# Kernel tuning notes

Measured on AMD Instinct MI355X. Metric: run time of the kernel, lower is better.

## Reference

```python
import jax, jax.numpy as jnp
import numpy as np

N_NODES = 100000
N_EDGES = 1600000
IN_F = 128
HID_F = 128
OUT_F = 16
N_GRAPHS = 256


def setup_inputs() -> dict:
    key = jax.random.key(0)
    ks = jax.random.split(key, 6)
    x = jax.random.normal(ks[0], (N_NODES, IN_F), dtype=jnp.float32)
    W1 = jax.random.normal(ks[1], (IN_F, HID_F), dtype=jnp.float32) * (1.0 / np.sqrt(IN_F))
    b1 = jax.random.normal(ks[2], (HID_F,), dtype=jnp.float32) * 0.01
    W2 = jax.random.normal(ks[3], (HID_F, OUT_F), dtype=jnp.float32) * (1.0 / np.sqrt(HID_F))
    b2 = jax.random.normal(ks[4], (OUT_F,), dtype=jnp.float32) * 0.01
    edge_index = jax.random.randint(ks[5], (2, N_EDGES), 0, N_NODES, dtype=jnp.int32)
    # sorted segment ids covering all graphs (~N/G nodes per graph, none empty)
    batch = ((jnp.arange(N_NODES, dtype=jnp.int64) * N_GRAPHS) // N_NODES).astype(jnp.int32)
    return {"x": x, "W1": W1, "b1": b1, "W2": W2, "b2": b2,
            "edge_index": edge_index, "batch": batch, "num_graphs": N_GRAPHS}


def gcn_conv(x, W, b, edge_index):
    # PyG GCNConv: h = x @ W; add self-loops; norm = deg^-1/2[src] * deg^-1/2[dst];
    # out[dst] += norm * h[src]; out += bias
    n = x.shape[0]
    h = x @ W  # [N, H]
    loop = jnp.arange(n, dtype=edge_index.dtype)
    src = jnp.concatenate([edge_index[0], loop])
    dst = jnp.concatenate([edge_index[1], loop])
    deg = jax.ops.segment_sum(jnp.ones_like(dst, dtype=h.dtype), dst, num_segments=n)
    dinv = jnp.where(deg > 0, jax.lax.rsqrt(jnp.maximum(deg, 1.0)), 0.0)
    norm = dinv[src] * dinv[dst]  # [E+N]
    msg = h[src] * norm[:, None]  # gather + scale
    out = jax.ops.segment_sum(msg, dst, num_segments=n)  # scatter-add
    return out + b


def reference(x, W1, b1, W2, b2, edge_index, batch, num_graphs):
    h = gcn_conv(x, W1, b1, edge_index)
    h = jax.nn.relu(h)
    pooled = jax.ops.segment_max(h, batch, num_segments=num_graphs)  # global max pool
    logits = pooled @ W2 + b2
    return jax.nn.log_softmax(logits, axis=-1)
```

## Files before the change

### kernel.cpp

```cpp
#include <hip/hip_runtime.h>

#define N_NODES 100000
#define N_EDGES 1600000
#define FDIM 128
#define OUTF 16
#define NGRAPH 256

#define NBLK 256
#define CHUNK 6250
#define NB_BUCKET 391
#define BC_N (NB_BUCKET * NBLK)
#define BC_SCAN_NB 98

typedef unsigned int uint;
typedef unsigned short ushort;
typedef short bf16x8 __attribute__((ext_vector_type(8)));
typedef float f32x4 __attribute__((ext_vector_type(4)));

__device__ inline uint pack_bf16(float a, float b) {
    uint ua = __float_as_uint(a); ua = (ua + 0x7fffu + ((ua >> 16) & 1u)) >> 16;
    uint ub = __float_as_uint(b); ub = (ub + 0x7fffu + ((ub >> 16) & 1u)) >> 16;
    return ua | (ub << 16);
}
__device__ inline ushort bf16_1(float a) {
    uint u = __float_as_uint(a);
    return (ushort)((u + 0x7fffu + ((u >> 16) & 1u)) >> 16);
}
__device__ inline void unpack_bf16(uint v, float& a, float& b) {
    a = __uint_as_float(v << 16);
    b = __uint_as_float(v & 0xffff0000u);
}

__launch_bounds__(256)
__global__ void k_bhist(const int* __restrict__ dst, int* __restrict__ bcount,
                        float* __restrict__ pooled, int* __restrict__ row_start,
                        const float* __restrict__ W, ushort* __restrict__ wt) {
    __shared__ int hist[NB_BUCKET];
    int t = threadIdx.x, blk = blockIdx.x;
    int gi = blk * 256 + t;
    if (gi < NGRAPH * FDIM) pooled[gi] = 0.0f;
    if (gi < FDIM * FDIM) {
        int col = gi >> 7, k = gi & 127;
        wt[col * 128 + k] = bf16_1(W[k * 128 + col]);
    }
    if (gi == 0) row_start[N_NODES] = N_EDGES;
    for (int i = t; i < NB_BUCKET; i += 256) hist[i] = 0;
    __syncthreads();
    int base = blk * CHUNK;
    for (int j = t; j < CHUNK; j += 256) atomicAdd(&hist[dst[base + j] >> 8], 1);
    __syncthreads();
    for (int i = t; i < NB_BUCKET; i += 256) bcount[i * NBLK + blk] = hist[i];
}

__global__ void k_scan1g(const int* __restrict__ in, int* __restrict__ offs,
                         int* __restrict__ bsums, int n) {
    __shared__ int tmp[256];
    int t = threadIdx.x;
    int base = blockIdx.x * 1024 + t * 4;
    int c[4]; int s = 0;
#pragma unroll
    for (int j = 0; j < 4; ++j) { c[j] = (base + j < n) ? in[base + j] : 0; s += c[j]; }
    tmp[t] = s; __syncthreads();
    for (int off = 1; off < 256; off <<= 1) {
        int v = (t >= off) ? tmp[t - off] : 0;
        __syncthreads();
        tmp[t] += v;
        __syncthreads();
    }
    int run = tmp[t] - s;
#pragma unroll
    for (int j = 0; j < 4; ++j) { if (base + j < n) offs[base + j] = run; run += c[j]; }
    if (t == 255) bsums[blockIdx.x] = tmp[255];
}

__global__ void k_scan2g(int* __restrict__ bsums, int* __restrict__ offs,
                         int nb, int n, int total) {
    if (threadIdx.x == 0) {
        int acc = 0;
        for (int i = 0; i < nb; ++i) { int v = bsums[i]; bsums[i] = acc; acc += v; }
        offs[n] = total;
    }
}

__global__ void k_scan3g(int* __restrict__ offs, const int* __restrict__ bsums, int n) {
    int t = threadIdx.x;
    int base = blockIdx.x * 1024 + t * 4;
    int add = bsums[blockIdx.x];
#pragma unroll
    for (int j = 0; j < 4; ++j) if (base + j < n) offs[base + j] += add;
}

__launch_bounds__(256)
__global__ void k_bucket(const int* __restrict__ src, const int* __restrict__ dst,
                         const int* __restrict__ boff, uint* __restrict__ ebuf) {
    __shared__ int cur[NB_BUCKET];
    int t = threadIdx.x, blk = blockIdx.x;
    for (int i = t; i < NB_BUCKET; i += 256) cur[i] = boff[i * NBLK + blk];
    __syncthreads();
    int base = blk * CHUNK;
    for (int j = t; j < CHUNK; j += 256) {
        int d = dst[base + j], s = src[base + j];
        int pos = atomicAdd(&cur[d >> 8], 1);
        ebuf[pos] = ((uint)(d & 255) << 17) | (uint)s;
    }
}

__launch_bounds__(256)
__global__ void k_build(const uint* __restrict__ ebuf, const int* __restrict__ boff,
                        int* __restrict__ row_start, float* __restrict__ dinv,
                        int* __restrict__ csr_src) {
    __shared__ int cnt[256], sh[256], cur[256];
    int t = threadIdx.x, b = blockIdx.x;
    int bstart = boff[b * NBLK];
    int bend   = boff[(b + 1) * NBLK];
    cnt[t] = 0;
    __syncthreads();
    for (int j = bstart + t; j < bend; j += 256)
        atomicAdd(&cnt[ebuf[j] >> 17], 1);
    __syncthreads();
    int c = cnt[t];
    sh[t] = c;
    __syncthreads();
    for (int o = 1; o < 256; o <<= 1) {
        int v = (t >= o) ? sh[t - o] : 0;
        __syncthreads();
        sh[t] += v;
        __syncthreads();
    }
    int rs = bstart + sh[t] - c;
    cur[t] = rs;
    int node = b * 256 + t;
    if (node < N_NODES) {
        row_start[node] = rs;
        dinv[node] = rsqrtf((float)c + 1.0f);
    }
    __syncthreads();
    for (int j = bstart + t; j < bend; j += 256) {
        uint e = ebuf[j];
        int pos = atomicAdd(&cur[e >> 17], 1);
        csr_src[pos] = (int)(e & 0x1FFFFu);
    }
}

#define BM 128
#define LDP 136
__launch_bounds__(256)
__global__ void k_gemm(const float* __restrict__ x, const ushort* __restrict__ wt,
                       const float* __restrict__ dinv, ushort* __restrict__ hbf) {
    __shared__ ushort AL[BM][LDP];
    __shared__ ushort WL[128][LDP];
    int t = threadIdx.x;
    int r0 = blockIdx.x * BM;

    for (int i = t; i < 128 * 16; i += 256) {
        int r = i >> 4, s = i & 15;
        *(uint4*)&WL[r][s * 8] = *(const uint4*)&wt[r * 128 + s * 8];
    }
    {
        int r = t >> 1, half = t & 1;
        int grow = r0 + r; if (grow >= N_NODES) grow = N_NODES - 1;
        const float4* xp = (const float4*)(x + (long)grow * FDIM + half * 64);
        ushort* ap = &AL[r][half * 64];
#pragma unroll
        for (int i = 0; i < 16; ++i) {
            float4 v = xp[i];
            uint2 p;
            p.x = pack_bf16(v.x, v.y);
            p.y = pack_bf16(v.z, v.w);
            *(uint2*)&ap[i * 4] = p;
        }
    }
    __syncthreads();

    int w = t >> 6, l = t & 63;
    int lr = l & 15;
    int lk = (l >> 4) * 8;
    f32x4 acc[2][8] = {};
#pragma unroll
    for (int kc = 0; kc < 4; ++kc) {
        int ko = kc * 32 + lk;
        bf16x8 a0 = *(const bf16x8*)&AL[w * 32 + lr][ko];
        bf16x8 a1 = *(const bf16x8*)&AL[w * 32 + 16 + lr][ko];
        bf16x8 b[8];
#pragma unroll
        for (int ct = 0; ct < 8; ++ct) b[ct] = *(const bf16x8*)&WL[ct * 16 + lr][ko];
#pragma unroll
        for (int ct = 0; ct < 8; ++ct) {
            acc[0][ct] = __builtin_amdgcn_mfma_f32_16x16x32_bf16(a0, b[ct], acc[0][ct], 0, 0, 0);
            acc[1][ct] = __builtin_amdgcn_mfma_f32_16x16x32_bf16(a1, b[ct], acc[1][ct], 0, 0, 0);
        }
    }
    int rbase = r0 + w * 32 + (l >> 4) * 4;
#pragma unroll
    for (int rt = 0; rt < 2; ++rt) {
#pragma unroll
        for (int reg = 0; reg < 4; ++reg) {
            int row = rbase + rt * 16 + reg;
            if (row < N_NODES) {
                float dv = dinv[row];
#pragma unroll
                for (int ct = 0; ct < 8; ++ct)
                    hbf[(long)row * FDIM + ct * 16 + lr] = bf16_1(dv * acc[rt][ct][reg]);
            }
        }
    }
}

__launch_bounds__(256)
__global__ void k_agg(const ushort* __restrict__ hbf, const float* __restrict__ dinv,
                      const int* __restrict__ row_start, const int* __restrict__ csr_src,
                      const float* __restrict__ b1, ushort* __restrict__ outbf) {
    int t = threadIdx.x;
    int lane = t & 31;
    int node = blockIdx.x * 8 + (t >> 5);
    const uint2* hb = (const uint2*)hbf;
    uint2 v = hb[node * 32 + lane];
    float s0, s1, s2, s3;
    unpack_bf16(v.x, s0, s1); unpack_bf16(v.y, s2, s3);
    int beg = row_start[node], end = row_start[node + 1];
    int j = beg;
    for (; j + 3 < end; j += 4) {
        uint2 va = hb[csr_src[j] * 32 + lane];
        uint2 vb = hb[csr_src[j + 1] * 32 + lane];
        uint2 vc = hb[csr_src[j + 2] * 32 + lane];
        uint2 vd = hb[csr_src[j + 3] * 32 + lane];
        float a0, a1, a2, a3;
        unpack_bf16(va.x, a0, a1); unpack_bf16(va.y, a2, a3);
        s0 += a0; s1 += a1; s2 += a2; s3 += a3;
        unpack_bf16(vb.x, a0, a1); unpack_bf16(vb.y, a2, a3);
        s0 += a0; s1 += a1; s2 += a2; s3 += a3;
        unpack_bf16(vc.x, a0, a1); unpack_bf16(vc.y, a2, a3);
        s0 += a0; s1 += a1; s2 += a2; s3 += a3;
        unpack_bf16(vd.x, a0, a1); unpack_bf16(vd.y, a2, a3);
        s0 += a0; s1 += a1; s2 += a2; s3 += a3;
    }
    for (; j < end; ++j) {
        uint2 va = hb[csr_src[j] * 32 + lane];
        float a0, a1, a2, a3;
        unpack_bf16(va.x, a0, a1); unpack_bf16(va.y, a2, a3);
        s0 += a0; s1 += a1; s2 += a2; s3 += a3;
    }
    float dd = dinv[node];
    float4 bv = ((const float4*)b1)[lane];
    uint2 o;
    o.x = pack_bf16(dd * s0 + bv.x, dd * s1 + bv.y);
    o.y = pack_bf16(dd * s2 + bv.z, dd * s3 + bv.w);
    ((uint2*)outbf)[node * 32 + lane] = o;
}

#define PNODES 64
__global__ void k_pool2(const ushort* __restrict__ outbf, const int* __restrict__ batch,
                        float* __restrict__ pooled) {
    int f = threadIdx.x;
    int r0 = blockIdx.x * PNODES;
    if (r0 >= N_NODES) return;
    int end = r0 + PNODES; if (end > N_NODES) end = N_NODES;
    float m = 0.0f;
    int gcur = batch[r0];
    for (int i = r0; i < end; ++i) {
        int g = batch[i];
        if (g != gcur) {
            atomicMax((int*)&pooled[gcur * FDIM + f], __float_as_int(m));
            m = 0.0f; gcur = g;
        }
        uint u = outbf[(long)i * FDIM + f];
        m = fmaxf(m, __uint_as_float(u << 16));
    }
    atomicMax((int*)&pooled[gcur * FDIM + f], __float_as_int(m));
}

__global__ void k_head(const float* __restrict__ pooled, const float* __restrict__ W2,
                       const float* __restrict__ b2, float* __restrict__ out) {
    int g = blockIdx.x;
    int lane = threadIdx.x;
    int c = lane & 15;
    float acc = b2[c];
    for (int k = 0; k < FDIM; ++k) acc += pooled[g * FDIM + k] * W2[k * OUTF + c];
    float m = acc;
    for (int off = 1; off < 16; off <<= 1) m = fmaxf(m, __shfl_xor(m, off, 16));
    float s = expf(acc - m);
    for (int off = 1; off < 16; off <<= 1) s += __shfl_xor(s, off, 16);
    if (lane < 16) out[g * OUTF + c] = acc - m - logf(s);
}

extern "C" void kernel_launch(void* const* d_in, const int* in_sizes, int n_in,
                              void* d_out, int out_size, void* d_ws, size_t ws_size,
                              hipStream_t stream) {
    const float* x  = (const float*)d_in[0];
    const float* W1 = (const float*)d_in[1];
    const float* b1 = (const float*)d_in[2];
    const float* W2 = (const float*)d_in[3];
    const float* b2 = (const float*)d_in[4];
    const int* ei   = (const int*)d_in[5];
    const int* batch = (const int*)d_in[6];
    const int* src = ei;
    const int* dst = ei + N_EDGES;
    float* out = (float*)d_out;

    char* ws = (char*)d_ws;
    float*  dinv      = (float*) (ws + 0);
    int*    row_start = (int*)   (ws + 400000);
    float*  pooled    = (float*) (ws + 800064);
    int*    bcount    = (int*)   (ws + 931200);
    int*    boff      = (int*)   (ws + 1331648);
    int*    bsums     = (int*)   (ws + 1732096);
    int*    csr_src   = (int*)   (ws + 1732544);
    uint*   ebuf      = (uint*)  (ws + 8132544);
    ushort* hbf       = (ushort*)(ws + 14532544);
    ushort* outbf     = (ushort*)(ws + 40132544);
    ushort* wtbf      = (ushort*)(ws + 65732544);

    k_bhist  <<<NBLK, 256, 0, stream>>>(dst, bcount, pooled, row_start, W1, wtbf);
    k_scan1g <<<BC_SCAN_NB, 256, 0, stream>>>(bcount, boff, bsums, BC_N);
    k_scan2g <<<1, 64, 0, stream>>>(bsums, boff, BC_SCAN_NB, BC_N, N_EDGES);
    k_scan3g <<<BC_SCAN_NB, 256, 0, stream>>>(boff, bsums, BC_N);
    k_bucket <<<NBLK, 256, 0, stream>>>(src, dst, boff, ebuf);
    k_build  <<<NB_BUCKET, 256, 0, stream>>>(ebuf, boff, row_start, dinv, csr_src);
    k_gemm   <<<(N_NODES + BM - 1) / BM, 256, 0, stream>>>(x, wtbf, dinv, hbf);
    k_agg    <<<N_NODES / 8, 256, 0, stream>>>(hbf, dinv, row_start, csr_src, b1, outbf);
    k_pool2  <<<(N_NODES + PNODES - 1) / PNODES, FDIM, 0, stream>>>(outbf, batch, pooled);
    k_head   <<<NGRAPH, 64, 0, stream>>>(pooled, W2, b2, out);
}
```

Baseline: 276.1 us.

## Fuse max-pooling into aggregation kernel and widen gather loads to 16 bytes

The aggregation kernel now applies bias and ReLU, stages each block's 16 node rows in shared memory, and does a per-block segmented max followed by atomicMax into pooled. This removes the bf16 intermediate output buffer and the separate pooling kernel launch, along with its global write and read. Each node is now handled by 16 lanes using uint4 (8 bf16) loads instead of 32 lanes using uint2 loads. The cost is more atomics per graph, since blocks cover only 16 nodes, plus a block-wide sync and shared-memory traffic.

```diff
diff --git a/kernel.cpp b/kernel.cpp
--- a/kernel.cpp
+++ b/kernel.cpp
@@ -206,67 +206,86 @@
     }
 }
 
+#define AGN 16
 __launch_bounds__(256)
 __global__ void k_agg(const ushort* __restrict__ hbf, const float* __restrict__ dinv,
                       const int* __restrict__ row_start, const int* __restrict__ csr_src,
-                      const float* __restrict__ b1, ushort* __restrict__ outbf) {
+                      const float* __restrict__ b1, const int* __restrict__ batch,
+                      float* __restrict__ pooled) {
+    __shared__ float P[AGN][FDIM];
+    __shared__ int sb[AGN];
     int t = threadIdx.x;
-    int lane = t & 31;
-    int node = blockIdx.x * 8 + (t >> 5);
-    const uint2* hb = (const uint2*)hbf;
-    uint2 v = hb[node * 32 + lane];
-    float s0, s1, s2, s3;
+    int lane = t & 15;
+    int ni = t >> 4;
+    int r0 = blockIdx.x * AGN;
+    int node = r0 + ni;
+    if (t < AGN) sb[t] = batch[r0 + t];
+
+    const uint4* hb = (const uint4*)hbf;
+    uint4 v = hb[node * 16 + lane];
+    float s0, s1, s2, s3, s4, s5, s6, s7;
     unpack_bf16(v.x, s0, s1); unpack_bf16(v.y, s2, s3);
+    unpack_bf16(v.z, s4, s5); unpack_bf16(v.w, s6, s7);
     int beg = row_start[node], end = row_start[node + 1];
     int j = beg;
     for (; j + 3 < end; j += 4) {
-        uint2 va = hb[csr_src[j] * 32 + lane];
-        uint2 vb = hb[csr_src[j + 1] * 32 + lane];
-        uint2 vc = hb[csr_src[j + 2] * 32 + lane];
-        uint2 vd = hb[csr_src[j + 3] * 32 + lane];
-        float a0, a1, a2, a3;
-        unpack_bf16(va.x, a0, a1); unpack_bf16(va.y, a2, a3);
-        s0 += a0; s1 += a1; s2 += a2; s3 += a3;
-        unpack_bf16(vb.x, a0, a1); unpack_bf16(vb.y, a2, a3);
-        s0 += a0; s1 += a1; s2 += a2; s3 += a3;
-        unpack_bf16(vc.x, a0, a1); unpack_bf16(vc.y, a2, a3);
-        s0 += a0; s1 += a1; s2 += a2; s3 += a3;
-        unpack_bf16(vd.x, a0, a1); unpack_bf16(vd.y, a2, a3);
-        s0 += a0; s1 += a1; s2 += a2; s3 += a3;
+        uint4 va = hb[csr_src[j] * 16 + lane];
+        uint4 vb = hb[csr_src[j + 1] * 16 + lane];
+        uint4 vc = hb[csr_src[j + 2] * 16 + lane];
+        uint4 vd = hb[csr_src[j + 3] * 16 + lane];
+        float a0, a1;
+        unpack_bf16(va.x, a0, a1); s0 += a0; s1 += a1;
+        unpack_bf16(va.y, a0, a1); s2 += a0; s3 += a1;
+        unpack_bf16(va.z, a0, a1); s4 += a0; s5 += a1;
+        unpack_bf16(va.w, a0, a1); s6 += a0; s7 += a1;
+        unpack_bf16(vb.x, a0, a1); s0 += a0; s1 += a1;
+        unpack_bf16(vb.y, a0, a1); s2 += a0; s3 += a1;
+        unpack_bf16(vb.z, a0, a1); s4 += a0; s5 += a1;
+        unpack_bf16(vb.w, a0, a1); s6 += a0; s7 += a1;
+        unpack_bf16(vc.x, a0, a1); s0 += a0; s1 += a1;
+        unpack_bf16(vc.y, a0, a1); s2 += a0; s3 += a1;
+        unpack_bf16(vc.z, a0, a1); s4 += a0; s5 += a1;
+        unpack_bf16(vc.w, a0, a1); s6 += a0; s7 += a1;
+        unpack_bf16(vd.x, a0, a1); s0 += a0; s1 += a1;
+        unpack_bf16(vd.y, a0, a1); s2 += a0; s3 += a1;
+        unpack_bf16(vd.z, a0, a1); s4 += a0; s5 += a1;
+        unpack_bf16(vd.w, a0, a1); s6 += a0; s7 += a1;
     }
     for (; j < end; ++j) {
-        uint2 va = hb[csr_src[j] * 32 + lane];
-        float a0, a1, a2, a3;
-        unpack_bf16(va.x, a0, a1); unpack_bf16(va.y, a2, a3);
-        s0 += a0; s1 += a1; s2 += a2; s3 += a3;
+        uint4 va = hb[csr_src[j] * 16 + lane];
+        float a0, a1;
+        unpack_bf16(va.x, a0, a1); s0 += a0; s1 += a1;
+        unpack_bf16(va.y, a0, a1); s2 += a0; s3 += a1;
+        unpack_bf16(va.z, a0, a1); s4 += a0; s5 += a1;
+        unpack_bf16(va.w, a0, a1); s6 += a0; s7 += a1;
     }
     float dd = dinv[node];
-    float4 bv = ((const float4*)b1)[lane];
-    uint2 o;
-    o.x = pack_bf16(dd * s0 + bv.x, dd * s1 + bv.y);
-    o.y = pack_bf16(dd * s2 + bv.z, dd * s3 + bv.w);
-    ((uint2*)outbf)[node * 32 + lane] = o;
-}
-
-#define PNODES 64
-__global__ void k_pool2(const ushort* __restrict__ outbf, const int* __restrict__ batch,
-                        float* __restrict__ pooled) {
-    int f = threadIdx.x;
-    int r0 = blockIdx.x * PNODES;
-    if (r0 >= N_NODES) return;
-    int end = r0 + PNODES; if (end > N_NODES) end = N_NODES;
-    float m = 0.0f;
-    int gcur = batch[r0];
-    for (int i = r0; i < end; ++i) {
-        int g = batch[i];
-        if (g != gcur) {
-            atomicMax((int*)&pooled[gcur * FDIM + f], __float_as_int(m));
-            m = 0.0f; gcur = g;
+    const float4* b4 = (const float4*)b1;
+    float4 bva = b4[lane * 2], bvb = b4[lane * 2 + 1];
+    float* pr = &P[ni][lane * 8];
+    pr[0] = fmaxf(0.0f, dd * s0 + bva.x);
+    pr[1] = fmaxf(0.0f, dd * s1 + bva.y);
+    pr[2] = fmaxf(0.0f, dd * s2 + bva.z);
+    pr[3] = fmaxf(0.0f, dd * s3 + bva.w);
+    pr[4] = fmaxf(0.0f, dd * s4 + bvb.x);
+    pr[5] = fmaxf(0.0f, dd * s5 + bvb.y);
+    pr[6] = fmaxf(0.0f, dd * s6 + bvb.z);
+    pr[7] = fmaxf(0.0f, dd * s7 + bvb.w);
+    __syncthreads();
+    if (t < FDIM) {
+        float m = 0.0f;
+        int gcur = sb[0];
+#pragma unroll
+        for (int i = 0; i < AGN; ++i) {
+            int g = sb[i];
+            if (g != gcur) {
+                atomicMax((int*)&pooled[gcur * FDIM + t], __float_as_int(m));
+                m = 0.0f; gcur = g;
+            }
+            m = fmaxf(m, P[i][t]);
         }
-        uint u = outbf[(long)i * FDIM + f];
-        m = fmaxf(m, __uint_as_float(u << 16));
-    }
-    atomicMax((int*)&pooled[gcur * FDIM + f], __float_as_int(m));
+        atomicMax((int*)&pooled[gcur * FDIM + t], __float_as_int(m));
+    }
 }
 
 __global__ void k_head(const float* __restrict__ pooled, const float* __restrict__ W2,
@@ -307,8 +326,7 @@
     int*    csr_src   = (int*)   (ws + 1732544);
     uint*   ebuf      = (uint*)  (ws + 8132544);
     ushort* hbf       = (ushort*)(ws + 14532544);
-    ushort* outbf     = (ushort*)(ws + 40132544);
-    ushort* wtbf      = (ushort*)(ws + 65732544);
+    ushort* wtbf      = (ushort*)(ws + 40132544);
 
     k_bhist  <<<NBLK, 256, 0, stream>>>(dst, bcount, pooled, row_start, W1, wtbf);
     k_scan1g <<<BC_SCAN_NB, 256, 0, stream>>>(bcount, boff, bsums, BC_N);
@@ -317,7 +335,6 @@
     k_bucket <<<NBLK, 256, 0, stream>>>(src, dst, boff, ebuf);
     k_build  <<<NB_BUCKET, 256, 0, stream>>>(ebuf, boff, row_start, dinv, csr_src);
     k_gemm   <<<(N_NODES + BM - 1) / BM, 256, 0, stream>>>(x, wtbf, dinv, hbf);
-    k_agg    <<<N_NODES / 8, 256, 0, stream>>>(hbf, dinv, row_start, csr_src, b1, outbf);
-    k_pool2  <<<(N_NODES + PNODES - 1) / PNODES, FDIM, 0, stream>>>(outbf, batch, pooled);
+    k_agg    <<<N_NODES / AGN, 256, 0, stream>>>(hbf, dinv, row_start, csr_src, b1, batch, pooled);
     k_head   <<<NGRAPH, 64, 0, stream>>>(pooled, W2, b2, out);
 }
```

Result: faster. 252.8 us (-8.4%).
